# Kernel optimization log

Measured on AMD Instinct MI355X. Metric: run time of the kernel, lower is better.

The kernel has to match this reference:

```python
import jax, jax.numpy as jnp
import numpy as np

DIM = 768
DEC = 768
B, N = 8, 4096


def setup_inputs() -> dict:
    key = jax.random.key(0)
    ks = jax.random.split(key, 7)
    s_in = DIM ** -0.5
    s_dec = DEC ** -0.5
    return {
        "x": jax.random.normal(ks[0], (B, N, DIM), dtype=jnp.float32),
        "Wq": jax.random.normal(ks[1], (DIM, DEC), dtype=jnp.float32) * s_in,
        "Wk": jax.random.normal(ks[2], (DIM, DEC), dtype=jnp.float32) * s_in,
        "Wv": jax.random.normal(ks[3], (DIM, DEC), dtype=jnp.float32) * s_in,
        "Wr": jax.random.normal(ks[4], (DEC, DEC), dtype=jnp.float32) * s_dec,
        "alpha": jax.random.normal(ks[5], (DEC,), dtype=jnp.float32),
        "beta": jax.random.normal(ks[6], (DEC,), dtype=jnp.float32),
    }


def reference(x, Wq, Wk, Wv, Wr, alpha, beta):
    # x: [b, n, dim] -> q/k/v: [b, n, d]
    q = jnp.einsum('bni,id->bnd', x, Wq)
    k = jnp.einsum('bni,id->bnd', x, Wk)
    v = jnp.einsum('bni,id->bnd', x, Wv)
    scale = q.shape[-1] ** -0.5

    # additive attention over feature dim (softmax along d, as in source)
    alpha_w = jax.nn.softmax(q * alpha * scale, axis=-1)          # [b, n, d]
    global_q = jnp.sum(q * alpha_w, axis=1)                        # [b, d]

    p = global_q[:, None, :] * k                                   # [b, n, d]
    beta_w = jax.nn.softmax(p * beta * scale, axis=-1)             # [b, n, d]
    global_k = jnp.sum(p * beta_w, axis=1)                         # [b, d]

    kv = global_k[:, None, :] * v                                  # [b, n, d]
    out = jnp.einsum('bnd,de->bne', kv, Wr) + q                    # [b, n, d]
    return out
```

## Files before the change

kernel.cpp:

```cpp
#include <hip/hip_runtime.h>
#include <stdint.h>


#define NBATCH 8
#define SEQ 4096
#define KD 768
#define ROWS (NBATCH * SEQ)
#define NT 12

typedef __bf16 bf16x8 __attribute__((ext_vector_type(8)));
typedef float f32x4 __attribute__((ext_vector_type(4)));

__device__ __forceinline__ unsigned short f2bf(float f) {
    __bf16 h = (__bf16)f;
    return __builtin_bit_cast(unsigned short, h);
}

__device__ __forceinline__ void gload16(const void* g, void* l) {
    __builtin_amdgcn_global_load_lds((const __attribute__((address_space(1))) void*)g,
                                     (__attribute__((address_space(3))) void*)l, 16, 0, 0);
}


__global__ __launch_bounds__(256) void cvt_f32_bf16x8(const float* __restrict__ src,
                                                      unsigned short* __restrict__ dst, int n8) {
    int i = blockIdx.x * 256 + threadIdx.x;
    if (i >= n8) return;
    const float4* p = (const float4*)src + (size_t)i * 2;
    float4 a = p[0], b = p[1];
    union { unsigned short s[8]; uint4 u; } t;
    t.s[0] = f2bf(a.x); t.s[1] = f2bf(a.y); t.s[2] = f2bf(a.z); t.s[3] = f2bf(a.w);
    t.s[4] = f2bf(b.x); t.s[5] = f2bf(b.y); t.s[6] = f2bf(b.z); t.s[7] = f2bf(b.w);
    ((uint4*)dst)[i] = t.u;
}

__global__ __launch_bounds__(256) void transpose_to_bf16(const float* __restrict__ W,
                                                         unsigned short* __restrict__ WT) {
    __shared__ float tile[32][33];
    int tx = threadIdx.x & 31, tg = threadIdx.x >> 5;
    int bi = blockIdx.x * 32, bj = blockIdx.y * 32;
#pragma unroll
    for (int j = 0; j < 4; ++j) {
        int r = tg * 4 + j;
        tile[r][tx] = W[(size_t)(bi + r) * KD + bj + tx];
    }
    __syncthreads();
#pragma unroll
    for (int j = 0; j < 4; ++j) {
        int r = tg * 4 + j;
        WT[(size_t)(bj + r) * KD + bi + tx] = f2bf(tile[tx][r]);
    }
}


template <int LDC, bool F32OUT>
__device__ __forceinline__ void gemm_core(const unsigned short* __restrict__ A,
                                          const unsigned short* __restrict__ Bp,
                                          void* __restrict__ Cout,
                                          int m0, int n0, char* lds) {
    const int tid = threadIdx.x;
    const int lane = tid & 63, wave = tid >> 6;
    const int wr = wave >> 1, wc = wave & 1;
    const int hi = lane >> 4, lo = lane & 15;
    char* lA = lds;
    char* lB = lds + 98304;

    f32x4 acc[4][4] = {};

    const int colb = (tid * 16) & 127;
    const int row0 = tid >> 3;
    const int sc = colb ^ ((row0 & 7) << 4);
    const size_t ldb = (size_t)KD * 2;
    const char* sAg = (const char*)A + (size_t)(m0 + row0) * ldb + sc;
    const char* sBg = (const char*)Bp + (size_t)(n0 + row0) * ldb + sc;

    int offA[4][2], offB[4][2];
#pragma unroll
    for (int m = 0; m < 4; ++m) {
        int ra = wr * 64 + m * 16 + lo;
        int rb = wc * 64 + m * 16 + lo;
#pragma unroll
        for (int kk = 0; kk < 2; ++kk) {
            offA[m][kk] = ra * 128 + ((kk * 64 + hi * 16) ^ ((ra & 7) << 4));
            offB[m][kk] = rb * 128 + ((kk * 64 + hi * 16) ^ ((rb & 7) << 4));
        }
    }

#define STAGE(t)                                                              \
    {                                                                         \
        const char* ga = sAg + (t) * 128;                                     \
        const char* gb = sBg + (t) * 128;                                     \
        char* dA = lA + ((t) % 3) * 32768 + tid * 16;                         \
        char* dB = lB + ((t) % 3) * 16384 + tid * 16;                         \
        gload16(ga, dA);                                                      \
        gload16(ga + 64 * ldb, dA + 8192);                                    \
        gload16(ga + 128 * ldb, dA + 16384);                                  \
        gload16(ga + 192 * ldb, dA + 24576);                                  \
        gload16(gb, dB);                                                      \
        gload16(gb + 64 * ldb, dB + 8192);                                    \
    }

    STAGE(0);
    STAGE(1);
    asm volatile("s_waitcnt vmcnt(6)" ::: "memory");
    __builtin_amdgcn_s_barrier();
    __builtin_amdgcn_sched_barrier(0);

    for (int t = 0; t < NT; ++t) {
        if (t + 2 < NT) STAGE(t + 2);
        const char* cA = lA + (t % 3) * 32768;
        const char* cB = lB + (t % 3) * 16384;
        bf16x8 af[4][2], bv[4][2];
#pragma unroll
        for (int m = 0; m < 4; ++m)
#pragma unroll
            for (int kk = 0; kk < 2; ++kk) af[m][kk] = *(const bf16x8*)(cA + offA[m][kk]);
#pragma unroll
        for (int n = 0; n < 4; ++n)
#pragma unroll
            for (int kk = 0; kk < 2; ++kk) bv[n][kk] = *(const bf16x8*)(cB + offB[n][kk]);
        __builtin_amdgcn_s_setprio(1);
#pragma unroll
        for (int m = 0; m < 4; ++m)
#pragma unroll
            for (int n = 0; n < 4; ++n)
#pragma unroll
                for (int kk = 0; kk < 2; ++kk)
                    acc[m][n] = __builtin_amdgcn_mfma_f32_16x16x32_bf16(af[m][kk], bv[n][kk],
                                                                        acc[m][n], 0, 0, 0);
        __builtin_amdgcn_s_setprio(0);
        if (t + 2 < NT)
            asm volatile("s_waitcnt vmcnt(6)" ::: "memory");
        else
            asm volatile("s_waitcnt vmcnt(0)" ::: "memory");
        __builtin_amdgcn_s_barrier();
        __builtin_amdgcn_sched_barrier(0);
    }
#undef STAGE

    const int r0 = m0 + wr * 64 + hi * 4;
    const int c0 = n0 + wc * 64 + lo;
#pragma unroll
    for (int m = 0; m < 4; ++m)
#pragma unroll
        for (int n = 0; n < 4; ++n)
#pragma unroll
            for (int r = 0; r < 4; ++r) {
                size_t idx = (size_t)(r0 + m * 16 + r) * LDC + (c0 + n * 16);
                if (F32OUT) ((float*)Cout)[idx] = acc[m][n][r];
                else        ((unsigned short*)Cout)[idx] = f2bf(acc[m][n][r]);
            }
}

__device__ __forceinline__ int xcd_swz(int bid, int nwg) {
    int cpx = nwg >> 3;
    return (bid & 7) * cpx + (bid >> 3);
}

__global__ __launch_bounds__(512) void gemm_qk(const unsigned short* __restrict__ xb,
                                               const unsigned short* __restrict__ Wcat,
                                               unsigned short* __restrict__ C) {
    __shared__ char lds[147456];
    int wg = xcd_swz(blockIdx.y * gridDim.x + blockIdx.x, gridDim.x * gridDim.y);
    const int m0 = (wg / 12) * 256, n0 = (wg % 12) * 128;
    gemm_core<1536, false>(xb, Wcat, C, m0, n0, lds);
}

__global__ __launch_bounds__(512) void gemm_out_f32(const unsigned short* __restrict__ xb,
                                                    const unsigned short* __restrict__ W3T,
                                                    float* __restrict__ out) {
    __shared__ char lds[147456];
    int wg = xcd_swz(blockIdx.y * gridDim.x + blockIdx.x, gridDim.x * gridDim.y);
    const int by = wg / 6, bx = wg % 6;
    const unsigned short* Bp = W3T + (size_t)(by >> 4) * (KD * KD);
    gemm_core<KD, true>(xb, Bp, out, by * 256, bx * 128, lds);
}


__device__ __forceinline__ void gemm_tile_bk64(const unsigned short* __restrict__ A,
                                               const unsigned short* __restrict__ B,
                                               int m0, int n0, short* sA, short* sB,
                                               f32x4 acc[4][4]) {
    const int tid = threadIdx.x;
    const int lane = tid & 63;
    const int hi = lane >> 4;
    const int wr = (tid >> 7) & 1, wc = (tid >> 6) & 1;
    const f32x4 zero = {0.f, 0.f, 0.f, 0.f};
#pragma unroll
    for (int m = 0; m < 4; ++m)
#pragma unroll
        for (int n = 0; n < 4; ++n) acc[m][n] = zero;

    const int o0 = tid * 16;
    const int srow = o0 >> 7, scb = o0 & 127;
    const int sc = scb ^ ((srow & 7) << 4);
    const char* pA0 = (const char*)A + (size_t)(m0 + srow) * (KD * 2) + sc;
    const char* pB0 = (const char*)B + (size_t)(n0 + srow) * (KD * 2) + sc;
    char* lA0 = (char*)sA + o0;
    char* lB0 = (char*)sB + o0;
    const size_t sstep = (size_t)32 * (KD * 2);

    int offA[4][2], offB[4][2];
#pragma unroll
    for (int m = 0; m < 4; ++m) {
        int rowa = wr * 64 + m * 16 + (lane & 15);
        int rowb = wc * 64 + m * 16 + (lane & 15);
        int swa = (rowa & 7) << 4, swb = (rowb & 7) << 4;
#pragma unroll
        for (int kk = 0; kk < 2; ++kk) {
            offA[m][kk] = rowa * 128 + ((kk * 64 + hi * 16) ^ swa);
            offB[m][kk] = rowb * 128 + ((kk * 64 + hi * 16) ^ swb);
        }
    }

    for (int kt = 0; kt < KD * 2; kt += 128) {
        __syncthreads();
#pragma unroll
        for (int s = 0; s < 4; ++s) gload16(pA0 + s * sstep + kt, lA0 + s * 4096);
#pragma unroll
        for (int s = 0; s < 4; ++s) gload16(pB0 + s * sstep + kt, lB0 + s * 4096);
        __syncthreads();
#pragma unroll
        for (int kk = 0; kk < 2; ++kk) {
            bf16x8 af[4], bv[4];
#pragma unroll
            for (int m = 0; m < 4; ++m) af[m] = *(const bf16x8*)((const char*)sA + offA[m][kk]);
#pragma unroll
            for (int n = 0; n < 4; ++n) bv[n] = *(const bf16x8*)((const char*)sB + offB[n][kk]);
#pragma unroll
            for (int m = 0; m < 4; ++m)
#pragma unroll
                for (int n = 0; n < 4; ++n)
                    acc[m][n] = __builtin_amdgcn_mfma_f32_16x16x32_bf16(af[m], bv[n], acc[m][n], 0, 0, 0);
        }
    }
}

__global__ __launch_bounds__(256) void gemm_w3(const unsigned short* __restrict__ WrS,
                                               const unsigned short* __restrict__ Wvb,
                                               const float* __restrict__ Wq,
                                               unsigned short* __restrict__ W3T) {
    __shared__ short sA[128 * 64];
    __shared__ short sB[128 * 64];
    f32x4 acc[4][4];
    const int b = blockIdx.z;
    const unsigned short* A = WrS + (size_t)b * (KD * KD);
    unsigned short* out = W3T + (size_t)b * (KD * KD);
    const int m0 = blockIdx.y * 128, n0 = blockIdx.x * 128;
    gemm_tile_bk64(A, Wvb, m0, n0, sA, sB, acc);
    const int lane = threadIdx.x & 63;
    const int wr = (threadIdx.x >> 7) & 1, wc = (threadIdx.x >> 6) & 1;
    const int r0 = m0 + wr * 64 + ((lane >> 4) * 4);
    const int c0 = n0 + wc * 64 + (lane & 15);
#pragma unroll
    for (int m = 0; m < 4; ++m)
#pragma unroll
        for (int n = 0; n < 4; ++n)
#pragma unroll
            for (int r = 0; r < 4; ++r) {
                int row = r0 + m * 16 + r, col = c0 + n * 16;
                out[(size_t)row * KD + col] = f2bf(acc[m][n][r] + Wq[(size_t)col * KD + row]);
            }
}


#define SM_SCALE 0.03608439182435161f
#define LDQK 1536

__device__ __forceinline__ void unpack12(const unsigned short* rowp, int lane, float* q) {
    uint4 u = *(const uint4*)(rowp + lane * 8);
    uint2 v = *(const uint2*)(rowp + 512 + lane * 4);
    q[0] = __uint_as_float(u.x << 16);  q[1] = __uint_as_float(u.x & 0xffff0000u);
    q[2] = __uint_as_float(u.y << 16);  q[3] = __uint_as_float(u.y & 0xffff0000u);
    q[4] = __uint_as_float(u.z << 16);  q[5] = __uint_as_float(u.z & 0xffff0000u);
    q[6] = __uint_as_float(u.w << 16);  q[7] = __uint_as_float(u.w & 0xffff0000u);
    q[8] = __uint_as_float(v.x << 16);  q[9] = __uint_as_float(v.x & 0xffff0000u);
    q[10] = __uint_as_float(v.y << 16); q[11] = __uint_as_float(v.y & 0xffff0000u);
}

__device__ __forceinline__ void load12f(const float* base, int lane, float* o) {
    const float4* p0 = (const float4*)(base + lane * 8);
    float4 x0 = p0[0], x1 = p0[1];
    float4 x2 = *(const float4*)(base + 512 + lane * 4);
    o[0] = x0.x; o[1] = x0.y; o[2] = x0.z; o[3] = x0.w;
    o[4] = x1.x; o[5] = x1.y; o[6] = x1.z; o[7] = x1.w;
    o[8] = x2.x; o[9] = x2.y; o[10] = x2.z; o[11] = x2.w;
}

__device__ __forceinline__ void block_partial_store(float* acc, int lane, int wave,
                                                    float* part_dst) {
    __shared__ float buf[4][KD];
#pragma unroll
    for (int j = 0; j < 8; ++j) buf[wave][lane * 8 + j] = acc[j];
#pragma unroll
    for (int j = 0; j < 4; ++j) buf[wave][512 + lane * 4 + j] = acc[8 + j];
    __syncthreads();
#pragma unroll
    for (int d = threadIdx.x; d < KD; d += 256)
        part_dst[d] = buf[0][d] + buf[1][d] + buf[2][d] + buf[3][d];
}

__global__ __launch_bounds__(256) void reduce_gq_s1(const unsigned short* __restrict__ qk,
                                                    const float* __restrict__ alpha,
                                                    float* __restrict__ part) {
    const int b = blockIdx.y;
    const int lane = threadIdx.x & 63, wave = threadIdx.x >> 6;
    float al[12];
    load12f(alpha, lane, al);
    float acc[12];
#pragma unroll
    for (int j = 0; j < 12; ++j) acc[j] = 0.f;
    const int row0 = b * SEQ + blockIdx.x * 64 + wave * 16;
#pragma unroll 2
    for (int rr = 0; rr < 16; ++rr) {
        const unsigned short* rowp = qk + (size_t)(row0 + rr) * LDQK;
        float q[12], t[12];
        unpack12(rowp, lane, q);
        float mx = -1e30f;
#pragma unroll
        for (int j = 0; j < 12; ++j) { t[j] = q[j] * al[j] * SM_SCALE; mx = fmaxf(mx, t[j]); }
#pragma unroll
        for (int s = 32; s > 0; s >>= 1) mx = fmaxf(mx, __shfl_xor(mx, s));
        float sum = 0.f, e[12];
#pragma unroll
        for (int j = 0; j < 12; ++j) { e[j] = __expf(t[j] - mx); sum += e[j]; }
#pragma unroll
        for (int s = 32; s > 0; s >>= 1) sum += __shfl_xor(sum, s);
        float inv = 1.f / sum;
#pragma unroll
        for (int j = 0; j < 12; ++j) acc[j] += q[j] * e[j] * inv;
    }
    block_partial_store(acc, lane, wave, part + ((size_t)b * 64 + blockIdx.x) * KD);
}

__global__ __launch_bounds__(256) void reduce_gk_s1(const unsigned short* __restrict__ qk,
                                                    const float* __restrict__ gq,
                                                    const float* __restrict__ beta,
                                                    float* __restrict__ part) {
    const int b = blockIdx.y;
    const int lane = threadIdx.x & 63, wave = threadIdx.x >> 6;
    float bt[12], gv[12];
    load12f(beta, lane, bt);
    load12f(gq + b * KD, lane, gv);
    float acc[12];
#pragma unroll
    for (int j = 0; j < 12; ++j) acc[j] = 0.f;
    const int row0 = b * SEQ + blockIdx.x * 64 + wave * 16;
#pragma unroll 2
    for (int rr = 0; rr < 16; ++rr) {
        const unsigned short* rowp = qk + (size_t)(row0 + rr) * LDQK + KD;
        float k[12], p[12], t[12];
        unpack12(rowp, lane, k);
        float mx = -1e30f;
#pragma unroll
        for (int j = 0; j < 12; ++j) {
            p[j] = gv[j] * k[j];
            t[j] = p[j] * bt[j] * SM_SCALE;
            mx = fmaxf(mx, t[j]);
        }
#pragma unroll
        for (int s = 32; s > 0; s >>= 1) mx = fmaxf(mx, __shfl_xor(mx, s));
        float sum = 0.f, e[12];
#pragma unroll
        for (int j = 0; j < 12; ++j) { e[j] = __expf(t[j] - mx); sum += e[j]; }
#pragma unroll
        for (int s = 32; s > 0; s >>= 1) sum += __shfl_xor(sum, s);
        float inv = 1.f / sum;
#pragma unroll
        for (int j = 0; j < 12; ++j) acc[j] += p[j] * e[j] * inv;
    }
    block_partial_store(acc, lane, wave, part + ((size_t)b * 64 + blockIdx.x) * KD);
}

__global__ __launch_bounds__(256) void reduce_s2(const float* __restrict__ part,
                                                 float* __restrict__ g) {
    const int b = blockIdx.y;
    const int d = blockIdx.x * 256 + threadIdx.x;
    const float* p = part + (size_t)b * 64 * KD + d;
    float s = 0.f;
#pragma unroll 8
    for (int i = 0; i < 64; ++i) s += p[(size_t)i * KD];
    g[b * KD + d] = s;
}

__global__ __launch_bounds__(256) void scale_wr(const unsigned short* __restrict__ WrT,
                                                const float* __restrict__ gk,
                                                unsigned short* __restrict__ WrS) {
    int i = blockIdx.x * 256 + threadIdx.x;
    const int per = (KD * KD) / 8;
    int b = i / per, g = i % per;
    int d = (g % (KD / 8)) * 8;
    uint4 w = *((const uint4*)WrT + g);
    const float* gkb = gk + b * KD + d;
    float4 s0 = *(const float4*)gkb;
    float4 s1 = *((const float4*)gkb + 1);
    union { unsigned short s[8]; uint4 u; } o;
    o.s[0] = f2bf(__uint_as_float(w.x << 16) * s0.x);
    o.s[1] = f2bf(__uint_as_float(w.x & 0xffff0000u) * s0.y);
    o.s[2] = f2bf(__uint_as_float(w.y << 16) * s0.z);
    o.s[3] = f2bf(__uint_as_float(w.y & 0xffff0000u) * s0.w);
    o.s[4] = f2bf(__uint_as_float(w.z << 16) * s1.x);
    o.s[5] = f2bf(__uint_as_float(w.z & 0xffff0000u) * s1.y);
    o.s[6] = f2bf(__uint_as_float(w.w << 16) * s1.z);
    o.s[7] = f2bf(__uint_as_float(w.w & 0xffff0000u) * s1.w);
    ((uint4*)WrS)[i] = o.u;
}


extern "C" void kernel_launch(void* const* d_in, const int* in_sizes, int n_in,
                              void* d_out, int out_size, void* d_ws, size_t ws_size,
                              hipStream_t stream) {
    const float* x     = (const float*)d_in[0];
    const float* Wq    = (const float*)d_in[1];
    const float* Wk    = (const float*)d_in[2];
    const float* Wv    = (const float*)d_in[3];
    const float* Wr    = (const float*)d_in[4];
    const float* alpha = (const float*)d_in[5];
    const float* beta  = (const float*)d_in[6];
    float* out = (float*)d_out;
    char* ws = (char*)d_ws;

    unsigned short* xb   = (unsigned short*)(ws);
    unsigned short* qk   = (unsigned short*)(ws + 50331648);
    unsigned short* Wcat = (unsigned short*)(ws + 150994944);
    unsigned short* WrT  = (unsigned short*)(ws + 153354240);
    unsigned short* Wvb  = (unsigned short*)(ws + 154533888);
    unsigned short* WrS  = (unsigned short*)(ws + 155713536);
    unsigned short* W3T  = (unsigned short*)(ws + 165150720);
    float* gq    = (float*)(ws + 174587904);
    float* gk    = (float*)(ws + 174612480);
    float* part1 = (float*)(ws + 174637056);
    float* part2 = (float*)(ws + 176209920);

    cvt_f32_bf16x8<<<12288, 256, 0, stream>>>(x, xb, (ROWS * KD) / 8);
    transpose_to_bf16<<<dim3(24, 24), 256, 0, stream>>>(Wq, Wcat);
    transpose_to_bf16<<<dim3(24, 24), 256, 0, stream>>>(Wk, Wcat + KD * KD);
    transpose_to_bf16<<<dim3(24, 24), 256, 0, stream>>>(Wr, WrT);
    cvt_f32_bf16x8<<<288, 256, 0, stream>>>(Wv, Wvb, (KD * KD) / 8);

    gemm_qk<<<dim3(12, 128), 512, 0, stream>>>(xb, Wcat, qk);
    reduce_gq_s1<<<dim3(64, NBATCH), 256, 0, stream>>>(qk, alpha, part1);
    reduce_s2<<<dim3(3, NBATCH), 256, 0, stream>>>(part1, gq);
    reduce_gk_s1<<<dim3(64, NBATCH), 256, 0, stream>>>(qk, gq, beta, part2);
    reduce_s2<<<dim3(3, NBATCH), 256, 0, stream>>>(part2, gk);

    scale_wr<<<2304, 256, 0, stream>>>(WrT, gk, WrS);
    gemm_w3<<<dim3(6, 6, NBATCH), 256, 0, stream>>>(WrS, Wvb, Wq, W3T);
    gemm_out_f32<<<dim3(6, 128), 512, 0, stream>>>(xb, W3T, out);
}
```

Measured before the change: 400.1 us.

## Merge weight prep kernels, fold reductions into consumers, reuse pipelined GEMM core

Folds the four weight-prep launches into one grid-z-indexed kernel. The second-stage reductions move into the consuming kernels (reduce_gk_s1 and a new sum_scale), which cuts four launches. gemm_w3 now uses the shared triple-buffered 256x128 GEMM core with an added epilogue mode, and the core's MFMA loop is split into two k-groups with a per-wave staggered k order to spread LDS bank access. The trade-off is redundant partial-sum work: each of the 64 gk blocks and 24 scale blocks re-reduces the partials.

```diff
diff --git a/kernel.cpp b/kernel.cpp
--- a/kernel.cpp
+++ b/kernel.cpp
@@ -34,29 +34,46 @@
     ((uint4*)dst)[i] = t.u;
 }
 
-__global__ __launch_bounds__(256) void transpose_to_bf16(const float* __restrict__ W,
-                                                         unsigned short* __restrict__ WT) {
+__global__ __launch_bounds__(256) void prep_w(const float* __restrict__ Wq,
+                                              const float* __restrict__ Wk,
+                                              const float* __restrict__ Wr,
+                                              const float* __restrict__ Wv,
+                                              unsigned short* __restrict__ Wcat,
+                                              unsigned short* __restrict__ WrT,
+                                              unsigned short* __restrict__ Wvb) {
     __shared__ float tile[32][33];
+    const int z = blockIdx.z;
+    const float* src = (z == 0) ? Wq : (z == 1) ? Wk : (z == 2) ? Wr : Wv;
+    unsigned short* dst = (z == 0) ? Wcat : (z == 1) ? (Wcat + KD * KD) : (z == 2) ? WrT : Wvb;
     int tx = threadIdx.x & 31, tg = threadIdx.x >> 5;
     int bi = blockIdx.x * 32, bj = blockIdx.y * 32;
+    if (z == 3) {
+#pragma unroll
+        for (int j = 0; j < 4; ++j) {
+            int r = bi + tg * 4 + j;
+            dst[(size_t)r * KD + bj + tx] = f2bf(src[(size_t)r * KD + bj + tx]);
+        }
+        return;
+    }
 #pragma unroll
     for (int j = 0; j < 4; ++j) {
         int r = tg * 4 + j;
-        tile[r][tx] = W[(size_t)(bi + r) * KD + bj + tx];
+        tile[r][tx] = src[(size_t)(bi + r) * KD + bj + tx];
     }
     __syncthreads();
 #pragma unroll
     for (int j = 0; j < 4; ++j) {
         int r = tg * 4 + j;
-        WT[(size_t)(bj + r) * KD + bi + tx] = f2bf(tile[tx][r]);
-    }
-}
-
-
-template <int LDC, bool F32OUT>
+        dst[(size_t)(bj + r) * KD + bi + tx] = f2bf(tile[tx][r]);
+    }
+}
+
+
+template <int LDC, int EPI>
 __device__ __forceinline__ void gemm_core(const unsigned short* __restrict__ A,
                                           const unsigned short* __restrict__ Bp,
                                           void* __restrict__ Cout,
+                                          const float* __restrict__ Wqp,
                                           int m0, int n0, char* lds) {
     const int tid = threadIdx.x;
     const int lane = tid & 63, wave = tid >> 6;
@@ -74,15 +91,17 @@
     const char* sAg = (const char*)A + (size_t)(m0 + row0) * ldb + sc;
     const char* sBg = (const char*)Bp + (size_t)(n0 + row0) * ldb + sc;
 
-    int offA[4][2], offB[4][2];
-#pragma unroll
-    for (int m = 0; m < 4; ++m) {
-        int ra = wr * 64 + m * 16 + lo;
-        int rb = wc * 64 + m * 16 + lo;
-#pragma unroll
-        for (int kk = 0; kk < 2; ++kk) {
-            offA[m][kk] = ra * 128 + ((kk * 64 + hi * 16) ^ ((ra & 7) << 4));
-            offB[m][kk] = rb * 128 + ((kk * 64 + hi * 16) ^ ((rb & 7) << 4));
+    const int kksel = wave & 1;
+    int offA[2][4], offB[2][4];
+#pragma unroll
+    for (int g = 0; g < 2; ++g) {
+        const int kkg = kksel ^ g;
+#pragma unroll
+        for (int m = 0; m < 4; ++m) {
+            int ra = wr * 64 + m * 16 + lo;
+            int rb = wc * 64 + m * 16 + lo;
+            offA[g][m] = ra * 128 + ((kkg * 64 + hi * 16) ^ ((ra & 7) << 4));
+            offB[g][m] = rb * 128 + ((kkg * 64 + hi * 16) ^ ((rb & 7) << 4));
         }
     }
 
@@ -110,25 +129,22 @@
         if (t + 2 < NT) STAGE(t + 2);
         const char* cA = lA + (t % 3) * 32768;
         const char* cB = lB + (t % 3) * 16384;
-        bf16x8 af[4][2], bv[4][2];
-#pragma unroll
-        for (int m = 0; m < 4; ++m)
-#pragma unroll
-            for (int kk = 0; kk < 2; ++kk) af[m][kk] = *(const bf16x8*)(cA + offA[m][kk]);
-#pragma unroll
-        for (int n = 0; n < 4; ++n)
-#pragma unroll
-            for (int kk = 0; kk < 2; ++kk) bv[n][kk] = *(const bf16x8*)(cB + offB[n][kk]);
-        __builtin_amdgcn_s_setprio(1);
-#pragma unroll
-        for (int m = 0; m < 4; ++m)
-#pragma unroll
-            for (int n = 0; n < 4; ++n)
-#pragma unroll
-                for (int kk = 0; kk < 2; ++kk)
-                    acc[m][n] = __builtin_amdgcn_mfma_f32_16x16x32_bf16(af[m][kk], bv[n][kk],
+#pragma unroll
+        for (int g = 0; g < 2; ++g) {
+            bf16x8 af[4], bv[4];
+#pragma unroll
+            for (int m = 0; m < 4; ++m) af[m] = *(const bf16x8*)(cA + offA[g][m]);
+#pragma unroll
+            for (int n = 0; n < 4; ++n) bv[n] = *(const bf16x8*)(cB + offB[g][n]);
+            __builtin_amdgcn_s_setprio(1);
+#pragma unroll
+            for (int m = 0; m < 4; ++m)
+#pragma unroll
+                for (int n = 0; n < 4; ++n)
+                    acc[m][n] = __builtin_amdgcn_mfma_f32_16x16x32_bf16(af[m], bv[n],
                                                                         acc[m][n], 0, 0, 0);
-        __builtin_amdgcn_s_setprio(0);
+            __builtin_amdgcn_s_setprio(0);
+        }
         if (t + 2 < NT)
             asm volatile("s_waitcnt vmcnt(6)" ::: "memory");
         else
@@ -146,9 +162,16 @@
         for (int n = 0; n < 4; ++n)
 #pragma unroll
             for (int r = 0; r < 4; ++r) {
-                size_t idx = (size_t)(r0 + m * 16 + r) * LDC + (c0 + n * 16);
-                if (F32OUT) ((float*)Cout)[idx] = acc[m][n][r];
-                else        ((unsigned short*)Cout)[idx] = f2bf(acc[m][n][r]);
+                int row = r0 + m * 16 + r, col = c0 + n * 16;
+                size_t idx = (size_t)row * LDC + col;
+                if (EPI == 1) {
+                    ((float*)Cout)[idx] = acc[m][n][r];
+                } else if (EPI == 2) {
+                    ((unsigned short*)Cout)[idx] =
+                        f2bf(acc[m][n][r] + Wqp[(size_t)col * KD + row]);
+                } else {
+                    ((unsigned short*)Cout)[idx] = f2bf(acc[m][n][r]);
+                }
             }
 }
 
@@ -162,8 +185,17 @@
                                                unsigned short* __restrict__ C) {
     __shared__ char lds[147456];
     int wg = xcd_swz(blockIdx.y * gridDim.x + blockIdx.x, gridDim.x * gridDim.y);
-    const int m0 = (wg / 12) * 256, n0 = (wg % 12) * 128;
-    gemm_core<1536, false>(xb, Wcat, C, m0, n0, lds);
+    gemm_core<1536, 0>(xb, Wcat, C, nullptr, (wg / 12) * 256, (wg % 12) * 128, lds);
+}
+
+__global__ __launch_bounds__(512) void gemm_w3(const unsigned short* __restrict__ WrS,
+                                               const unsigned short* __restrict__ Wvb,
+                                               const float* __restrict__ Wq,
+                                               unsigned short* __restrict__ W3T) {
+    __shared__ char lds[147456];
+    const int b = blockIdx.z;
+    gemm_core<KD, 2>(WrS + (size_t)b * (KD * KD), Wvb, W3T + (size_t)b * (KD * KD), Wq,
+                     blockIdx.y * 256, blockIdx.x * 128, lds);
 }
 
 __global__ __launch_bounds__(512) void gemm_out_f32(const unsigned short* __restrict__ xb,
@@ -173,94 +205,7 @@
     int wg = xcd_swz(blockIdx.y * gridDim.x + blockIdx.x, gridDim.x * gridDim.y);
     const int by = wg / 6, bx = wg % 6;
     const unsigned short* Bp = W3T + (size_t)(by >> 4) * (KD * KD);
-    gemm_core<KD, true>(xb, Bp, out, by * 256, bx * 128, lds);
-}
-
-
-__device__ __forceinline__ void gemm_tile_bk64(const unsigned short* __restrict__ A,
-                                               const unsigned short* __restrict__ B,
-                                               int m0, int n0, short* sA, short* sB,
-                                               f32x4 acc[4][4]) {
-    const int tid = threadIdx.x;
-    const int lane = tid & 63;
-    const int hi = lane >> 4;
-    const int wr = (tid >> 7) & 1, wc = (tid >> 6) & 1;
-    const f32x4 zero = {0.f, 0.f, 0.f, 0.f};
-#pragma unroll
-    for (int m = 0; m < 4; ++m)
-#pragma unroll
-        for (int n = 0; n < 4; ++n) acc[m][n] = zero;
-
-    const int o0 = tid * 16;
-    const int srow = o0 >> 7, scb = o0 & 127;
-    const int sc = scb ^ ((srow & 7) << 4);
-    const char* pA0 = (const char*)A + (size_t)(m0 + srow) * (KD * 2) + sc;
-    const char* pB0 = (const char*)B + (size_t)(n0 + srow) * (KD * 2) + sc;
-    char* lA0 = (char*)sA + o0;
-    char* lB0 = (char*)sB + o0;
-    const size_t sstep = (size_t)32 * (KD * 2);
-
-    int offA[4][2], offB[4][2];
-#pragma unroll
-    for (int m = 0; m < 4; ++m) {
-        int rowa = wr * 64 + m * 16 + (lane & 15);
-        int rowb = wc * 64 + m * 16 + (lane & 15);
-        int swa = (rowa & 7) << 4, swb = (rowb & 7) << 4;
-#pragma unroll
-        for (int kk = 0; kk < 2; ++kk) {
-            offA[m][kk] = rowa * 128 + ((kk * 64 + hi * 16) ^ swa);
-            offB[m][kk] = rowb * 128 + ((kk * 64 + hi * 16) ^ swb);
-        }
-    }
-
-    for (int kt = 0; kt < KD * 2; kt += 128) {
-        __syncthreads();
-#pragma unroll
-        for (int s = 0; s < 4; ++s) gload16(pA0 + s * sstep + kt, lA0 + s * 4096);
-#pragma unroll
-        for (int s = 0; s < 4; ++s) gload16(pB0 + s * sstep + kt, lB0 + s * 4096);
-        __syncthreads();
-#pragma unroll
-        for (int kk = 0; kk < 2; ++kk) {
-            bf16x8 af[4], bv[4];
-#pragma unroll
-            for (int m = 0; m < 4; ++m) af[m] = *(const bf16x8*)((const char*)sA + offA[m][kk]);
-#pragma unroll
-            for (int n = 0; n < 4; ++n) bv[n] = *(const bf16x8*)((const char*)sB + offB[n][kk]);
-#pragma unroll
-            for (int m = 0; m < 4; ++m)
-#pragma unroll
-                for (int n = 0; n < 4; ++n)
-                    acc[m][n] = __builtin_amdgcn_mfma_f32_16x16x32_bf16(af[m], bv[n], acc[m][n], 0, 0, 0);
-        }
-    }
-}
-
-__global__ __launch_bounds__(256) void gemm_w3(const unsigned short* __restrict__ WrS,
-                                               const unsigned short* __restrict__ Wvb,
-                                               const float* __restrict__ Wq,
-                                               unsigned short* __restrict__ W3T) {
-    __shared__ short sA[128 * 64];
-    __shared__ short sB[128 * 64];
-    f32x4 acc[4][4];
-    const int b = blockIdx.z;
-    const unsigned short* A = WrS + (size_t)b * (KD * KD);
-    unsigned short* out = W3T + (size_t)b * (KD * KD);
-    const int m0 = blockIdx.y * 128, n0 = blockIdx.x * 128;
-    gemm_tile_bk64(A, Wvb, m0, n0, sA, sB, acc);
-    const int lane = threadIdx.x & 63;
-    const int wr = (threadIdx.x >> 7) & 1, wc = (threadIdx.x >> 6) & 1;
-    const int r0 = m0 + wr * 64 + ((lane >> 4) * 4);
-    const int c0 = n0 + wc * 64 + (lane & 15);
-#pragma unroll
-    for (int m = 0; m < 4; ++m)
-#pragma unroll
-        for (int n = 0; n < 4; ++n)
-#pragma unroll
-            for (int r = 0; r < 4; ++r) {
-                int row = r0 + m * 16 + r, col = c0 + n * 16;
-                out[(size_t)row * KD + col] = f2bf(acc[m][n][r] + Wq[(size_t)col * KD + row]);
-            }
+    gemm_core<KD, 1>(xb, Bp, out, nullptr, by * 256, bx * 128, lds);
 }
 
 
@@ -334,14 +279,30 @@
 }
 
 __global__ __launch_bounds__(256) void reduce_gk_s1(const unsigned short* __restrict__ qk,
-                                                    const float* __restrict__ gq,
+                                                    const float* __restrict__ part1,
                                                     const float* __restrict__ beta,
                                                     float* __restrict__ part) {
+    __shared__ float sgq[KD];
     const int b = blockIdx.y;
     const int lane = threadIdx.x & 63, wave = threadIdx.x >> 6;
+    {
+        const float* p = part1 + (size_t)b * 64 * KD;
+#pragma unroll
+        for (int j = 0; j < 3; ++j) {
+            int d = threadIdx.x + j * 256;
+            float s = 0.f;
+#pragma unroll 8
+            for (int i = 0; i < 64; ++i) s += p[(size_t)i * KD + d];
+            sgq[d] = s;
+        }
+    }
+    __syncthreads();
     float bt[12], gv[12];
     load12f(beta, lane, bt);
-    load12f(gq + b * KD, lane, gv);
+#pragma unroll
+    for (int j = 0; j < 8; ++j) gv[j] = sgq[lane * 8 + j];
+#pragma unroll
+    for (int j = 0; j < 4; ++j) gv[8 + j] = sgq[512 + lane * 4 + j];
     float acc[12];
 #pragma unroll
     for (int j = 0; j < 12; ++j) acc[j] = 0.f;
@@ -372,38 +333,42 @@
     block_partial_store(acc, lane, wave, part + ((size_t)b * 64 + blockIdx.x) * KD);
 }
 
-__global__ __launch_bounds__(256) void reduce_s2(const float* __restrict__ part,
-                                                 float* __restrict__ g) {
+__global__ __launch_bounds__(256) void sum_scale(const float* __restrict__ part2,
+                                                 const unsigned short* __restrict__ WrT,
+                                                 unsigned short* __restrict__ WrS) {
+    __shared__ float sgk[KD];
     const int b = blockIdx.y;
-    const int d = blockIdx.x * 256 + threadIdx.x;
-    const float* p = part + (size_t)b * 64 * KD + d;
-    float s = 0.f;
+    {
+        const float* p = part2 + (size_t)b * 64 * KD;
+#pragma unroll
+        for (int j = 0; j < 3; ++j) {
+            int d = threadIdx.x + j * 256;
+            float s = 0.f;
 #pragma unroll 8
-    for (int i = 0; i < 64; ++i) s += p[(size_t)i * KD];
-    g[b * KD + d] = s;
-}
-
-__global__ __launch_bounds__(256) void scale_wr(const unsigned short* __restrict__ WrT,
-                                                const float* __restrict__ gk,
-                                                unsigned short* __restrict__ WrS) {
-    int i = blockIdx.x * 256 + threadIdx.x;
-    const int per = (KD * KD) / 8;
-    int b = i / per, g = i % per;
-    int d = (g % (KD / 8)) * 8;
-    uint4 w = *((const uint4*)WrT + g);
-    const float* gkb = gk + b * KD + d;
-    float4 s0 = *(const float4*)gkb;
-    float4 s1 = *((const float4*)gkb + 1);
-    union { unsigned short s[8]; uint4 u; } o;
-    o.s[0] = f2bf(__uint_as_float(w.x << 16) * s0.x);
-    o.s[1] = f2bf(__uint_as_float(w.x & 0xffff0000u) * s0.y);
-    o.s[2] = f2bf(__uint_as_float(w.y << 16) * s0.z);
-    o.s[3] = f2bf(__uint_as_float(w.y & 0xffff0000u) * s0.w);
-    o.s[4] = f2bf(__uint_as_float(w.z << 16) * s1.x);
-    o.s[5] = f2bf(__uint_as_float(w.z & 0xffff0000u) * s1.y);
-    o.s[6] = f2bf(__uint_as_float(w.w << 16) * s1.z);
-    o.s[7] = f2bf(__uint_as_float(w.w & 0xffff0000u) * s1.w);
-    ((uint4*)WrS)[i] = o.u;
+            for (int i = 0; i < 64; ++i) s += p[(size_t)i * KD + d];
+            sgk[d] = s;
+        }
+    }
+    __syncthreads();
+    const int e0 = blockIdx.x * 32;
+    unsigned short* dst = WrS + (size_t)b * (KD * KD);
+#pragma unroll
+    for (int c = 0; c < 12; ++c) {
+        int idx = c * 256 + threadIdx.x;
+        int row = e0 + (idx / 96);
+        int col = (idx % 96) * 8;
+        uint4 w = *(const uint4*)(WrT + (size_t)row * KD + col);
+        union { unsigned short s[8]; uint4 u; } o;
+        o.s[0] = f2bf(__uint_as_float(w.x << 16) * sgk[col + 0]);
+        o.s[1] = f2bf(__uint_as_float(w.x & 0xffff0000u) * sgk[col + 1]);
+        o.s[2] = f2bf(__uint_as_float(w.y << 16) * sgk[col + 2]);
+        o.s[3] = f2bf(__uint_as_float(w.y & 0xffff0000u) * sgk[col + 3]);
+        o.s[4] = f2bf(__uint_as_float(w.z << 16) * sgk[col + 4]);
+        o.s[5] = f2bf(__uint_as_float(w.z & 0xffff0000u) * sgk[col + 5]);
+        o.s[6] = f2bf(__uint_as_float(w.w << 16) * sgk[col + 6]);
+        o.s[7] = f2bf(__uint_as_float(w.w & 0xffff0000u) * sgk[col + 7]);
+        *(uint4*)(dst + (size_t)row * KD + col) = o.u;
+    }
 }
 
 
@@ -427,24 +392,17 @@
     unsigned short* Wvb  = (unsigned short*)(ws + 154533888);
     unsigned short* WrS  = (unsigned short*)(ws + 155713536);
     unsigned short* W3T  = (unsigned short*)(ws + 165150720);
-    float* gq    = (float*)(ws + 174587904);
-    float* gk    = (float*)(ws + 174612480);
     float* part1 = (float*)(ws + 174637056);
     float* part2 = (float*)(ws + 176209920);
 
     cvt_f32_bf16x8<<<12288, 256, 0, stream>>>(x, xb, (ROWS * KD) / 8);
-    transpose_to_bf16<<<dim3(24, 24), 256, 0, stream>>>(Wq, Wcat);
-    transpose_to_bf16<<<dim3(24, 24), 256, 0, stream>>>(Wk, Wcat + KD * KD);
-    transpose_to_bf16<<<dim3(24, 24), 256, 0, stream>>>(Wr, WrT);
-    cvt_f32_bf16x8<<<288, 256, 0, stream>>>(Wv, Wvb, (KD * KD) / 8);
+    prep_w<<<dim3(24, 24, 4), 256, 0, stream>>>(Wq, Wk, Wr, Wv, Wcat, WrT, Wvb);
 
     gemm_qk<<<dim3(12, 128), 512, 0, stream>>>(xb, Wcat, qk);
     reduce_gq_s1<<<dim3(64, NBATCH), 256, 0, stream>>>(qk, alpha, part1);
-    reduce_s2<<<dim3(3, NBATCH), 256, 0, stream>>>(part1, gq);
-    reduce_gk_s1<<<dim3(64, NBATCH), 256, 0, stream>>>(qk, gq, beta, part2);
-    reduce_s2<<<dim3(3, NBATCH), 256, 0, stream>>>(part2, gk);
-
-    scale_wr<<<2304, 256, 0, stream>>>(WrT, gk, WrS);
-    gemm_w3<<<dim3(6, 6, NBATCH), 256, 0, stream>>>(WrS, Wvb, Wq, W3T);
+    reduce_gk_s1<<<dim3(64, NBATCH), 256, 0, stream>>>(qk, part1, beta, part2);
+
+    sum_scale<<<dim3(24, NBATCH), 256, 0, stream>>>(part2, WrT, WrS);
+    gemm_w3<<<dim3(6, 3, NBATCH), 512, 0, stream>>>(WrS, Wvb, Wq, W3T);
     gemm_out_f32<<<dim3(6, 128), 512, 0, stream>>>(xb, W3T, out);
 }
```

Result: no change. 393.5 us (-1.6%).
